# Optimization experiments

Hardware: AMD Instinct MI355X
Metric: run time of the kernel (lower is better)

The kernel has to match this reference:

```python
import jax, jax.numpy as jnp
import numpy as np

N = 50000; E = 200000; H = 128; L = 3; T = 2; FOUT = 64
G = 1000; NP = 3; ATOM_V = 64; BOND_V = 8
EPS = 1e-5
_DEG_HIST = np.array([0., 50000., 75000., 50000., 25000.])
# PyG PNAConv: avg_deg['log'] = sum(hist[d] * log(d+1)) / num_nodes
AVG_DEG_LOG = float((np.log(np.arange(5) + 1.0) * _DEG_HIST).sum() / _DEG_HIST.sum())


def _bn(v, g, b):
    # training-mode BatchNorm1d (biased variance), eps=1e-5
    mu = v.mean(0)
    var = ((v - mu) ** 2).mean(0)
    return (v - mu) * jax.lax.rsqrt(var + EPS) * g + b


def setup_inputs() -> dict:
    key = jax.random.key(0)
    ks = jax.random.split(key, 16)
    def nrm(k, shape, fan):
        return (jax.random.normal(k, shape, dtype=jnp.float32) / np.sqrt(fan)).astype(jnp.float32)
    return {
        'x': jax.random.randint(ks[0], (N, 9), 0, ATOM_V),
        'edge_index': jax.random.randint(ks[1], (2, E), 0, N),
        'batch': jnp.sort(jax.random.randint(ks[2], (N,), 0, G)),
        'edge_attr_idx': jax.random.randint(ks[3], (E, 3), 0, BOND_V),
        'atom_emb': nrm(ks[4], (9, ATOM_V, H), H),
        'bond_emb': nrm(ks[5], (3, BOND_V, H), H),
        'edge_W': nrm(ks[6], (L, H, H), H), 'edge_b': jnp.zeros((L, H), jnp.float32),
        'pre_W': nrm(ks[7], (L, T, 3 * H, H), 3 * H), 'pre_b': jnp.zeros((L, T, H), jnp.float32),
        'post_W': nrm(ks[8], (L, T, 13 * H, FOUT), 13 * H), 'post_b': jnp.zeros((L, T, FOUT), jnp.float32),
        'lin_W': nrm(ks[9], (L, H, H), H), 'lin_b': jnp.zeros((L, H), jnp.float32),
        'bn_g': jnp.ones((L, H), jnp.float32), 'bn_b': jnp.zeros((L, H), jnp.float32),
        'mlp_W': nrm(ks[10], (2, H, H), H), 'mlp_b': jnp.zeros((2, H), jnp.float32),
        'mlp_g': jnp.ones((2, H), jnp.float32), 'mlp_be': jnp.zeros((2, H), jnp.float32),
        'hW1': nrm(ks[11], (H, H // 2), H), 'hb1': jnp.zeros((H // 2,), jnp.float32),
        'hg1': jnp.ones((H // 2,), jnp.float32), 'hbe1': jnp.zeros((H // 2,), jnp.float32),
        'hW2': nrm(ks[12], (H // 2, H // 4), H // 2), 'hb2': jnp.zeros((H // 4,), jnp.float32),
        'hg2': jnp.ones((H // 4,), jnp.float32), 'hbe2': jnp.zeros((H // 4,), jnp.float32),
        'hW3': nrm(ks[13], (H // 4, NP), H // 4), 'hb3': jnp.zeros((NP,), jnp.float32),
    }


def reference(x, edge_index, batch, edge_attr_idx, atom_emb, bond_emb,
              edge_W, edge_b, pre_W, pre_b, post_W, post_b, lin_W, lin_b,
              bn_g, bn_b, mlp_W, mlp_b, mlp_g, mlp_be,
              hW1, hb1, hg1, hbe1, hW2, hb2, hg2, hbe2, hW3, hb3):
    # encoders: sum of per-feature embeddings (OGB Atom/Bond encoder)
    h = atom_emb[jnp.arange(9), x].sum(1)               # [N,H]
    e = bond_emb[jnp.arange(3), edge_attr_idx].sum(1)   # [E,H]
    src, dst = edge_index[0], edge_index[1]
    cnt = jax.ops.segment_sum(jnp.ones((E,), jnp.float32), dst, N)
    deg = jnp.maximum(cnt, 1.0)[:, None, None]          # clamp(1), as in PyG scalers
    amp = jnp.log(deg + 1.0) / AVG_DEG_LOG
    att = AVG_DEG_LOG / jnp.log(deg + 1.0)
    has = (cnt > 0)[:, None, None]
    for l in range(L):
        ea = e @ edge_W[l] + edge_b[l]                                  # [E,H]
        msg_in = jnp.concatenate([h[dst], h[src], ea], -1)              # [E,3H]
        m = jnp.einsum('ef,tfh->eth', msg_in, pre_W[l]) + pre_b[l]      # [E,T,H]
        s1 = jax.ops.segment_sum(m, dst, N)
        s2 = jax.ops.segment_sum(m * m, dst, N)
        mean = s1 / deg
        std = jnp.sqrt(jax.nn.relu(s2 / deg - mean * mean) + EPS)
        mn = jnp.where(has, jax.ops.segment_min(m, dst, N), 0.0)
        mx = jnp.where(has, jax.ops.segment_max(m, dst, N), 0.0)
        agg = jnp.concatenate([mean, mn, mx, std], -1)                  # [N,T,4H]
        scaled = jnp.concatenate([agg, agg * amp, agg * att], -1)       # [N,T,12H]
        upd = jnp.concatenate(
            [jnp.broadcast_to(h[:, None, :], (N, T, H)), scaled], -1)   # [N,T,13H]
        o = jnp.einsum('ntf,tfo->nto', upd, post_W[l]) + post_b[l]      # [N,T,FOUT]
        o = o.reshape(N, T * FOUT) @ lin_W[l] + lin_b[l]                # [N,H]
        h = jax.nn.relu(_bn(o, bn_g[l], bn_b[l]))
    g = jax.ops.segment_sum(h, batch, G)                                # [G,H]
    for i in range(2):
        g = jax.nn.relu(_bn(g @ mlp_W[i] + mlp_b[i], mlp_g[i], mlp_be[i]))
    g = jax.nn.relu(_bn(g @ hW1 + hb1, hg1, hbe1))
    g = jax.nn.relu(_bn(g @ hW2 + hb2, hg2, hbe2))
    return g @ hW3 + hb3                                                # [G,NP]
```

## Files before the change

kernel.cpp:

```cpp
#include <hip/hip_runtime.h>
#include <math.h>


#define NN 50000
#define NE 200000
#define HD 128
#define NG 1000
#define EPSV 1e-5f
#define ALOGC 1.1330197327247628f

#define AP 1288
#define OP 136
#define ECAP 512

typedef __bf16 bf16x8 __attribute__((ext_vector_type(8)));
typedef float f32x4 __attribute__((ext_vector_type(4)));

__device__ __forceinline__ unsigned short f2bf(float f) {
    unsigned int u = __float_as_uint(f);
    unsigned int r = (u + 0x7FFFu + ((u >> 16) & 1u)) >> 16;
    return (unsigned short)r;
}
__device__ __forceinline__ float bf2f(unsigned short h) {
    return __uint_as_float((unsigned int)h << 16);
}

__global__ void k_fill(float* __restrict__ o, float v, int n) {
    int i = blockIdx.x * 256 + threadIdx.x;
    if (i < n) o[i] = v;
}

__global__ void k_zero(float* __restrict__ z, int n) {
    int i = blockIdx.x * 256 + threadIdx.x;
    if (i < n) z[i] = 0.f;
}

__global__ void k_encode_nodes(const int* __restrict__ x, const float* __restrict__ aemb,
                               float* __restrict__ h) {
    int n = blockIdx.x, c = threadIdx.x;
    __shared__ int xi[9];
    if (c < 9) xi[c] = x[n * 9 + c];
    __syncthreads();
    float acc = 0.f;
#pragma unroll
    for (int f = 0; f < 9; ++f) acc += aemb[(f * 64 + xi[f]) * HD + c];
    h[(size_t)n * HD + c] = acc;
}

__global__ void k_count(const int* __restrict__ dst, int* __restrict__ cnt) {
    int e = blockIdx.x * 256 + threadIdx.x;
    if (e < NE) atomicAdd(&cnt[dst[e]], 1);
}

__global__ __launch_bounds__(1024) void k_scan(
    const int* __restrict__ cnt, int* __restrict__ rowptr,
    float* __restrict__ ampv, float* __restrict__ attv) {
    __shared__ int buf[1024];
    __shared__ int s_off;
    int tid = threadIdx.x;
    if (tid == 0) { s_off = 0; rowptr[0] = 0; }
    __syncthreads();
    for (int base = 0; base < NN; base += 1024) {
        int i = base + tid;
        int v = (i < NN) ? cnt[i] : 0;
        if (i < NN) {
            float dg = (float)(v > 0 ? v : 1);
            float lg = logf(dg + 1.0f);
            ampv[i] = lg / ALOGC;
            attv[i] = ALOGC / lg;
        }
        buf[tid] = v;
        __syncthreads();
        for (int s = 1; s < 1024; s <<= 1) {
            int t = (tid >= s) ? buf[tid - s] : 0;
            __syncthreads();
            buf[tid] += t;
            __syncthreads();
        }
        int off = s_off;
        if (i < NN) rowptr[i + 1] = off + buf[tid];
        __syncthreads();
        if (tid == 1023) s_off = off + buf[1023];
        __syncthreads();
    }
}

__global__ void k_scatter(const int* __restrict__ dst, const int* __restrict__ rowptr,
                          int* __restrict__ fill, int* __restrict__ eperm) {
    int e = blockIdx.x * 256 + threadIdx.x;
    if (e < NE) {
        int d = dst[e];
        int pos = rowptr[d] + atomicAdd(&fill[d], 1);
        eperm[pos] = e;
    }
}

__global__ void k_eprep(const int* __restrict__ ei, const int* __restrict__ eai,
                        const int* __restrict__ eperm,
                        int* __restrict__ psrc, int* __restrict__ pbnd) {
    int p = blockIdx.x * 256 + threadIdx.x;
    if (p < NE) {
        int e = eperm[p];
        psrc[p] = ei[e];
        pbnd[p] = eai[e * 3] | (eai[e * 3 + 1] << 4) | (eai[e * 3 + 2] << 8);
    }
}

__global__ void k_fold(const float* __restrict__ edge_W, const float* __restrict__ edge_b,
                       const float* __restrict__ pre_W, const float* __restrict__ pre_b,
                       float* __restrict__ cW, float* __restrict__ tb) {
    int l = blockIdx.y;
    int k = blockIdx.x;
    int tj = threadIdx.x;
    int t = tj >> 7, j = tj & 127;
    const float* pw = pre_W + ((size_t)(l * 2 + t) * 384 + 256) * 128 + j;
    if (k < 128) {
        const float* ew = edge_W + ((size_t)l * 128 + k) * 128;
        float acc = 0.f;
        for (int i = 0; i < 128; ++i) acc += ew[i] * pw[i * 128];
        cW[((size_t)l * 128 + k) * 256 + tj] = acc;
    } else {
        const float* eb = edge_b + l * 128;
        float acc = pre_b[(l * 2 + t) * 128 + j];
        for (int i = 0; i < 128; ++i) acc += eb[i] * pw[i * 128];
        tb[l * 256 + tj] = acc;
    }
}

__global__ void k_bond(const float* __restrict__ bemb, const float* __restrict__ cW,
                       float* __restrict__ bondc) {
    int v = blockIdx.x, f = blockIdx.y, l = blockIdx.z;
    int tj = threadIdx.x;
    const float* src = bemb + (size_t)(f * 8 + v) * 128;
    const float* w = cW + (size_t)l * 128 * 256;
    float acc = 0.f;
    for (int i = 0; i < 128; ++i) acc += src[i] * w[i * 256 + tj];
    bondc[(((size_t)l * 3 + f) * 8 + v) * 256 + tj] = acc;
}

__global__ void k_pack(const float* __restrict__ W, int N, int NT,
                       unsigned short* __restrict__ pk) {
    int blk = blockIdx.x;
    int kstep = blk / NT, nt = blk - kstep * NT;
    int lane = threadIdx.x;
    int kb = kstep * 32 + (lane >> 4) * 8;
    int col = nt * 16 + (lane & 15);
    unsigned short tmp[8];
#pragma unroll
    for (int i = 0; i < 8; ++i) tmp[i] = f2bf(W[(size_t)(kb + i) * N + col]);
    *(uint4*)(pk + ((size_t)blk * 64 + lane) * 8) = *(uint4*)tmp;
}

__global__ void k_pack_pre(const float* __restrict__ preW,
                           unsigned short* __restrict__ phi,
                           unsigned short* __restrict__ plo) {
    int b = blockIdx.x;
    int kstep = b >> 5, nt = b & 31;
    int lane = threadIdx.x;
    int q = lane >> 4, nc = lane & 15;
    int col = nt * 16 + nc;
    int t = (col >> 7) & 1;
    int jcol = col & 127;
    int fbase = (col < 256) ? 0 : 128;
    unsigned short hi[8], lo[8];
#pragma unroll
    for (int i = 0; i < 8; ++i) {
        int k = kstep * 32 + q * 8 + i;
        float w = preW[((size_t)t * 384 + fbase + k) * 128 + jcol];
        unsigned short h16 = f2bf(w);
        hi[i] = h16;
        lo[i] = f2bf(w - bf2f(h16));
    }
    size_t base = ((size_t)b * 64 + lane) * 8;
    *(uint4*)(phi + base) = *(uint4*)hi;
    *(uint4*)(plo + base) = *(uint4*)lo;
}

__global__ __launch_bounds__(256) void k_pre_m(
    const float* __restrict__ h,
    const unsigned short* __restrict__ phi, const unsigned short* __restrict__ plo,
    const float* __restrict__ tb,
    float* __restrict__ hz) {
    __shared__ __align__(16) unsigned short ah[16 * 136];
    __shared__ __align__(16) unsigned short al[16 * 136];
    int n0 = blockIdx.x * 16;
    int tid = threadIdx.x;
    {
        int node = tid >> 4, cg = (tid & 15) * 8;
        const float* hs = h + (size_t)(n0 + node) * HD + cg;
        float4 v0 = *(const float4*)(hs);
        float4 v1 = *(const float4*)(hs + 4);
        float vv[8] = {v0.x, v0.y, v0.z, v0.w, v1.x, v1.y, v1.z, v1.w};
        unsigned short hh[8], ll[8];
#pragma unroll
        for (int i = 0; i < 8; ++i) {
            hh[i] = f2bf(vv[i]);
            ll[i] = f2bf(vv[i] - bf2f(hh[i]));
        }
        *(uint4*)(ah + node * 136 + cg) = *(uint4*)hh;
        *(uint4*)(al + node * 136 + cg) = *(uint4*)ll;
    }
    __syncthreads();
    int lane = tid & 63, w = tid >> 6;
    int q = lane >> 4, nc = lane & 15;
    f32x4 acc[8];
#pragma unroll
    for (int j = 0; j < 8; ++j) acc[j] = (f32x4){0.f, 0.f, 0.f, 0.f};
#pragma unroll
    for (int kk = 0; kk < 4; ++kk) {
        bf16x8 Ahi = *(const bf16x8*)(ah + nc * 136 + kk * 32 + q * 8);
        bf16x8 Alo = *(const bf16x8*)(al + nc * 136 + kk * 32 + q * 8);
#pragma unroll
        for (int j = 0; j < 8; ++j) {
            int nt = w * 8 + j;
            size_t base = ((size_t)(kk * 32 + nt) * 64 + lane) * 8;
            bf16x8 Bhi = *(const bf16x8*)(phi + base);
            bf16x8 Blo = *(const bf16x8*)(plo + base);
            acc[j] = __builtin_amdgcn_mfma_f32_16x16x32_bf16(Ahi, Bhi, acc[j], 0, 0, 0);
            acc[j] = __builtin_amdgcn_mfma_f32_16x16x32_bf16(Ahi, Blo, acc[j], 0, 0, 0);
            acc[j] = __builtin_amdgcn_mfma_f32_16x16x32_bf16(Alo, Bhi, acc[j], 0, 0, 0);
        }
    }
#pragma unroll
    for (int j = 0; j < 8; ++j) {
        int col = (w * 8 + j) * 16 + nc;
        float bias = (col < 256) ? tb[col] : 0.f;
#pragma unroll
        for (int reg = 0; reg < 4; ++reg) {
            hz[(size_t)(n0 + q * 4 + reg) * 512 + col] = acc[j][reg] + bias;
        }
    }
}

__global__ __launch_bounds__(256) void k_post(
    const float* __restrict__ h, const float* __restrict__ hz,
    const int* __restrict__ rowptr,
    const int* __restrict__ psrc, const int* __restrict__ pbnd,
    const float* __restrict__ bondc,
    const float* __restrict__ ampv, const float* __restrict__ attv,
    const unsigned short* __restrict__ pkPost,
    const float* __restrict__ postb,
    const unsigned short* __restrict__ pkLin,
    const float* __restrict__ linb,
    float* __restrict__ o2, float* __restrict__ stats) {
    __shared__ __align__(16) unsigned short a_lds[16 * AP];
    __shared__ __align__(16) unsigned short o_lds[16 * OP];
    __shared__ int es_src[ECAP], es_bnd[ECAP];
    __shared__ float s_amp[16], s_att[16];
    int n0 = blockIdx.x * 16;
    int tid = threadIdx.x;

    int pbase = rowptr[n0];
    int ecount = rowptr[n0 + 16] - pbase;
    for (int i = tid; i < ecount && i < ECAP; i += 256) {
        es_src[i] = psrc[pbase + i];
        es_bnd[i] = pbnd[pbase + i];
    }
    {
        int node = tid >> 4, cg = (tid & 15) * 8;
        const float* hs = h + (size_t)(n0 + node) * HD + cg;
        float4 v0 = *(const float4*)(hs);
        float4 v1 = *(const float4*)(hs + 4);
        unsigned short* d0 = a_lds + node * AP + cg;
        unsigned short* d1 = d0 + 640;
        unsigned short b[8];
        b[0] = f2bf(v0.x); b[1] = f2bf(v0.y); b[2] = f2bf(v0.z); b[3] = f2bf(v0.w);
        b[4] = f2bf(v1.x); b[5] = f2bf(v1.y); b[6] = f2bf(v1.z); b[7] = f2bf(v1.w);
#pragma unroll
        for (int i = 0; i < 8; ++i) { d0[i] = b[i]; d1[i] = b[i]; }
    }
    if (tid < 16) { s_amp[tid] = ampv[n0 + tid]; s_att[tid] = attv[n0 + tid]; }
    __syncthreads();

    {
        int wv = tid >> 6, lane = tid & 63;
        int cc = lane * 4;
        int tt = cc >> 7, jj = cc & 127;
        const float* b0t = bondc;
        const float* b1t = bondc + 8 * 256;
        const float* b2t = bondc + 16 * 256;
        bool incap = (ecount <= ECAP);
        int nwb = n0 + wv * 4;
        int bnd[5];
        bnd[0] = rowptr[nwb];
        bnd[1] = rowptr[nwb + 1];
        bnd[2] = rowptr[nwb + 2];
        bnd[3] = rowptr[nwb + 3];
        bnd[4] = rowptr[nwb + 4];
        int e0 = bnd[0], e4 = bnd[4];
        float4 hd0 = *(const float4*)(hz + (size_t)(nwb + 0) * 512 + cc);
        float4 hd1 = *(const float4*)(hz + (size_t)(nwb + 1) * 512 + cc);
        float4 hd2 = *(const float4*)(hz + (size_t)(nwb + 2) * 512 + cc);
        float4 hd3 = *(const float4*)(hz + (size_t)(nwb + 3) * 512 + cc);
        float4 hd = hd0;
        const float4 Z4 = make_float4(0.f, 0.f, 0.f, 0.f);
        const float4 BIG4 = make_float4(3.4e38f, 3.4e38f, 3.4e38f, 3.4e38f);
        const float4 NBIG4 = make_float4(-3.4e38f, -3.4e38f, -3.4e38f, -3.4e38f);
        float4 s1 = Z4, s2 = Z4, mn = BIG4, mx = NBIG4;
        int ni = 0;

        auto fin = [&](int nloc) {
            int cnt = bnd[nloc + 1] - bnd[nloc];
            float inv = 1.f / (float)(cnt > 0 ? cnt : 1);
            float4 mean, stdv;
            mean.x = s1.x * inv; mean.y = s1.y * inv;
            mean.z = s1.z * inv; mean.w = s1.w * inv;
            stdv.x = sqrtf(fmaxf(s2.x * inv - mean.x * mean.x, 0.f) + EPSV);
            stdv.y = sqrtf(fmaxf(s2.y * inv - mean.y * mean.y, 0.f) + EPSV);
            stdv.z = sqrtf(fmaxf(s2.z * inv - mean.z * mean.z, 0.f) + EPSV);
            stdv.w = sqrtf(fmaxf(s2.w * inv - mean.w * mean.w, 0.f) + EPSV);
            if (cnt == 0) { mn = Z4; mx = Z4; }
            unsigned short* d = a_lds + (wv * 4 + nloc) * AP + tt * 640 + 128 + jj;
            d[0] = f2bf(mean.x); d[1] = f2bf(mean.y); d[2] = f2bf(mean.z); d[3] = f2bf(mean.w);
            d += 128; d[0] = f2bf(mn.x); d[1] = f2bf(mn.y); d[2] = f2bf(mn.z); d[3] = f2bf(mn.w);
            d += 128; d[0] = f2bf(mx.x); d[1] = f2bf(mx.y); d[2] = f2bf(mx.z); d[3] = f2bf(mx.w);
            d += 128; d[0] = f2bf(stdv.x); d[1] = f2bf(stdv.y); d[2] = f2bf(stdv.z); d[3] = f2bf(stdv.w);
            s1 = Z4; s2 = Z4; mn = BIG4; mx = NBIG4;
        };

        float4 vsn = Z4, q0n = Z4, q1n = Z4, q2n = Z4;
        if (e0 < e4) {
            int sp = incap ? es_src[e0 - pbase] : psrc[e0];
            int pb = incap ? es_bnd[e0 - pbase] : pbnd[e0];
            vsn = *(const float4*)(hz + (size_t)sp * 512 + 256 + cc);
            q0n = *(const float4*)(b0t + (pb & 15) * 256 + cc);
            q1n = *(const float4*)(b1t + ((pb >> 4) & 15) * 256 + cc);
            q2n = *(const float4*)(b2t + ((pb >> 8) & 15) * 256 + cc);
        }
        for (int p = e0; p < e4; ++p) {
            while (p == bnd[ni + 1]) {
                fin(ni);
                ++ni;
                hd = (ni == 1) ? hd1 : (ni == 2) ? hd2 : hd3;
            }
            float4 vs = vsn, q0 = q0n, q1 = q1n, q2 = q2n;
            int pn = p + 1;
            if (pn < e4) {
                int sp = incap ? es_src[pn - pbase] : psrc[pn];
                int pb = incap ? es_bnd[pn - pbase] : pbnd[pn];
                vsn = *(const float4*)(hz + (size_t)sp * 512 + 256 + cc);
                q0n = *(const float4*)(b0t + (pb & 15) * 256 + cc);
                q1n = *(const float4*)(b1t + ((pb >> 4) & 15) * 256 + cc);
                q2n = *(const float4*)(b2t + ((pb >> 8) & 15) * 256 + cc);
            }
            float vx = hd.x + vs.x + q0.x + q1.x + q2.x;
            float vy = hd.y + vs.y + q0.y + q1.y + q2.y;
            float vz = hd.z + vs.z + q0.z + q1.z + q2.z;
            float vw = hd.w + vs.w + q0.w + q1.w + q2.w;
            s1.x += vx; s1.y += vy; s1.z += vz; s1.w += vw;
            s2.x += vx * vx; s2.y += vy * vy; s2.z += vz * vz; s2.w += vw * vw;
            mn.x = fminf(mn.x, vx); mn.y = fminf(mn.y, vy);
            mn.z = fminf(mn.z, vz); mn.w = fminf(mn.w, vw);
            mx.x = fmaxf(mx.x, vx); mx.y = fmaxf(mx.y, vy);
            mx.z = fmaxf(mx.z, vz); mx.w = fmaxf(mx.w, vw);
        }
        while (ni < 4) { fin(ni); ++ni; }
    }
    __syncthreads();

    {
        int lane = tid & 63;
        int w = tid >> 6;
        int t = w >> 1;
        int ntb = (w & 1) * 2;
        int q = lane >> 4, nc = lane & 15;
        const unsigned short* arow = a_lds + (size_t)nc * AP + t * 640 + q * 8;
        const unsigned short* pkt = pkPost + (size_t)t * 106496;
        f32x4 aP0 = {0.f, 0.f, 0.f, 0.f}, aP1 = {0.f, 0.f, 0.f, 0.f};
        f32x4 aA0 = {0.f, 0.f, 0.f, 0.f}, aA1 = {0.f, 0.f, 0.f, 0.f};
        f32x4 aT0 = {0.f, 0.f, 0.f, 0.f}, aT1 = {0.f, 0.f, 0.f, 0.f};
        for (int kk = 0; kk < 20; ++kk) {
            bf16x8 af = *(const bf16x8*)(arow + kk * 32);
            const unsigned short* pb = pkt + ((size_t)(kk * 4 + ntb) * 64 + lane) * 8;
            aP0 = __builtin_amdgcn_mfma_f32_16x16x32_bf16(af, *(const bf16x8*)(pb), aP0, 0, 0, 0);
            aP1 = __builtin_amdgcn_mfma_f32_16x16x32_bf16(af, *(const bf16x8*)(pb + 512), aP1, 0, 0, 0);
            if (kk >= 4) {
                const unsigned short* pa = pkt + ((size_t)((kk + 16) * 4 + ntb) * 64 + lane) * 8;
                aA0 = __builtin_amdgcn_mfma_f32_16x16x32_bf16(af, *(const bf16x8*)(pa), aA0, 0, 0, 0);
                aA1 = __builtin_amdgcn_mfma_f32_16x16x32_bf16(af, *(const bf16x8*)(pa + 512), aA1, 0, 0, 0);
                const unsigned short* pt = pkt + ((size_t)((kk + 32) * 4 + ntb) * 64 + lane) * 8;
                aT0 = __builtin_amdgcn_mfma_f32_16x16x32_bf16(af, *(const bf16x8*)(pt), aT0, 0, 0, 0);
                aT1 = __builtin_amdgcn_mfma_f32_16x16x32_bf16(af, *(const bf16x8*)(pt + 512), aT1, 0, 0, 0);
            }
        }
#pragma unroll
        for (int u = 0; u < 2; ++u) {
            int nt = ntb + u;
            int col = t * 64 + nt * 16 + nc;
            float pbia = postb[t * 64 + nt * 16 + nc];
            f32x4 P = u ? aP1 : aP0;
            f32x4 A = u ? aA1 : aA0;
            f32x4 T = u ? aT1 : aT0;
#pragma unroll
            for (int reg = 0; reg < 4; ++reg) {
                int mrow = q * 4 + reg;
                float val = P[reg] + s_amp[mrow] * A[reg] + s_att[mrow] * T[reg] + pbia;
                o_lds[mrow * OP + col] = f2bf(val);
            }
        }
    }
    __syncthreads();

    {
        int lane = tid & 63;
        int w = tid >> 6;
        int ntb = w * 2;
        int q = lane >> 4, nc = lane & 15;
        const unsigned short* arow = o_lds + (size_t)nc * OP + q * 8;
        f32x4 L0 = {0.f, 0.f, 0.f, 0.f}, L1 = {0.f, 0.f, 0.f, 0.f};
#pragma unroll
        for (int kk = 0; kk < 4; ++kk) {
            bf16x8 af = *(const bf16x8*)(arow + kk * 32);
            const unsigned short* pb = pkLin + ((size_t)(kk * 8 + ntb) * 64 + lane) * 8;
            L0 = __builtin_amdgcn_mfma_f32_16x16x32_bf16(af, *(const bf16x8*)(pb), L0, 0, 0, 0);
            L1 = __builtin_amdgcn_mfma_f32_16x16x32_bf16(af, *(const bf16x8*)(pb + 512), L1, 0, 0, 0);
        }
#pragma unroll
        for (int u = 0; u < 2; ++u) {
            int col = (ntb + u) * 16 + nc;
            float lb = linb[col];
            f32x4 L = u ? L1 : L0;
            float ps = 0.f, pss = 0.f;
#pragma unroll
            for (int reg = 0; reg < 4; ++reg) {
                int mrow = q * 4 + reg;
                float v = L[reg] + lb;
                o2[(size_t)(n0 + mrow) * HD + col] = v;
                ps += v; pss += v * v;
            }
            ps += __shfl_down(ps, 16); ps += __shfl_down(ps, 32);
            pss += __shfl_down(pss, 16); pss += __shfl_down(pss, 32);
            if (q == 0) {
                atomicAdd(&stats[col], ps);
                atomicAdd(&stats[128 + col], pss);
            }
        }
    }
}

__global__ void k_bn_relu(const float* __restrict__ o2, const float* __restrict__ stats,
                          const float* __restrict__ g, const float* __restrict__ b,
                          float* __restrict__ h) {
    int idx = blockIdx.x * 256 + threadIdx.x;
    int c = idx & 127;
    float mu = stats[c] * (1.f / NN);
    float var = stats[128 + c] * (1.f / NN) - mu * mu;
    float v = (o2[idx] - mu) * rsqrtf(var + EPSV) * g[c] + b[c];
    h[idx] = fmaxf(v, 0.f);
}

__global__ void k_pool(const float* __restrict__ h, const int* __restrict__ batch,
                       float* __restrict__ g0) {
    int c = threadIdx.x;
    int nbase = blockIdx.x * 64;
    float run = 0.f; int cur = -1;
    for (int i = 0; i < 64; ++i) {
        int n = nbase + i;
        if (n >= NN) break;
        int bb = batch[n];
        if (bb != cur) {
            if (cur >= 0) atomicAdd(&g0[(size_t)cur * HD + c], run);
            cur = bb; run = 0.f;
        }
        run += h[(size_t)n * HD + c];
    }
    if (cur >= 0) atomicAdd(&g0[(size_t)cur * HD + c], run);
}

__global__ void k_head_gemm(const float* __restrict__ x, const float* __restrict__ W,
                            const float* __restrict__ b, float* __restrict__ y,
                            float* __restrict__ stats, int K, int Kout) {
    int row = blockIdx.x;
    int col = threadIdx.x;
    if (col >= Kout) return;
    float acc = b[col];
    for (int k = 0; k < K; k += 4) {
        float4 xv = *(const float4*)(x + (size_t)row * K + k);
        acc += xv.x * W[(k + 0) * Kout + col] + xv.y * W[(k + 1) * Kout + col]
             + xv.z * W[(k + 2) * Kout + col] + xv.w * W[(k + 3) * Kout + col];
    }
    y[(size_t)row * Kout + col] = acc;
    if (stats) {
        atomicAdd(&stats[col], acc);
        atomicAdd(&stats[Kout + col], acc * acc);
    }
}

__global__ void k_head_bn(float* __restrict__ y, const float* __restrict__ stats,
                          const float* __restrict__ g, const float* __restrict__ b, int Kout) {
    int idx = blockIdx.x * 256 + threadIdx.x;
    if (idx >= NG * Kout) return;
    int c = idx % Kout;
    float mu = stats[c] * (1.f / NG);
    float var = stats[Kout + c] * (1.f / NG) - mu * mu;
    float v = (y[idx] - mu) * rsqrtf(var + EPSV) * g[c] + b[c];
    y[idx] = fmaxf(v, 0.f);
}

extern "C" void kernel_launch(void* const* d_in, const int* in_sizes, int n_in,
                              void* d_out, int out_size, void* d_ws, size_t ws_size,
                              hipStream_t stream) {
    const int*   x        = (const int*)  d_in[0];
    const int*   ei       = (const int*)  d_in[1];
    const int*   batch    = (const int*)  d_in[2];
    const int*   eai      = (const int*)  d_in[3];
    const float* atom_emb = (const float*)d_in[4];
    const float* bond_emb = (const float*)d_in[5];
    const float* edge_W   = (const float*)d_in[6];
    const float* edge_b   = (const float*)d_in[7];
    const float* pre_W    = (const float*)d_in[8];
    const float* pre_b    = (const float*)d_in[9];
    const float* post_W   = (const float*)d_in[10];
    const float* post_b   = (const float*)d_in[11];
    const float* lin_W    = (const float*)d_in[12];
    const float* lin_b    = (const float*)d_in[13];
    const float* bn_g     = (const float*)d_in[14];
    const float* bn_b     = (const float*)d_in[15];
    const float* mlp_W    = (const float*)d_in[16];
    const float* mlp_b    = (const float*)d_in[17];
    const float* mlp_g    = (const float*)d_in[18];
    const float* mlp_be   = (const float*)d_in[19];
    const float* hW1 = (const float*)d_in[20]; const float* hb1  = (const float*)d_in[21];
    const float* hg1 = (const float*)d_in[22]; const float* hbe1 = (const float*)d_in[23];
    const float* hW2 = (const float*)d_in[24]; const float* hb2  = (const float*)d_in[25];
    const float* hg2 = (const float*)d_in[26]; const float* hbe2 = (const float*)d_in[27];
    const float* hW3 = (const float*)d_in[28]; const float* hb3  = (const float*)d_in[29];
    float* out = (float*)d_out;
    (void)n_in; (void)in_sizes;

    char* p = (char*)d_ws;
    size_t off = 0;
    auto alloc = [&](size_t bytes) -> char* {
        char* r = p + off;
        off += (bytes + 255) & ~(size_t)255;
        return r;
    };
    float* h     = (float*)alloc((size_t)NN * HD * 4);
    float* o2    = (float*)alloc((size_t)NN * HD * 4);
    float* hz    = (float*)alloc((size_t)NN * 512 * 4);
    float* ampv  = (float*)alloc((size_t)NN * 4);
    float* attv  = (float*)alloc((size_t)NN * 4);
    int*   rowptr= (int*)  alloc((size_t)(NN + 1) * 4);
    int*   eperm = (int*)  alloc((size_t)NE * 4);
    int*   psrc  = (int*)  alloc((size_t)NE * 4);
    int*   pbnd  = (int*)  alloc((size_t)NE * 4);
    float* cW    = (float*)alloc((size_t)3 * 128 * 256 * 4);
    float* tbb   = (float*)alloc((size_t)3 * 256 * 4);
    float* bondc = (float*)alloc((size_t)3 * 3 * 8 * 256 * 4);
    unsigned short* pkPost  = (unsigned short*)alloc((size_t)3 * 2 * 106496 * 2);
    unsigned short* pkLin   = (unsigned short*)alloc((size_t)3 * 16384 * 2);
    unsigned short* pkPreHi = (unsigned short*)alloc((size_t)3 * 65536 * 2);
    unsigned short* pkPreLo = (unsigned short*)alloc((size_t)3 * 65536 * 2);
    float* gA    = (float*)alloc((size_t)NG * HD * 4);
    float* gB    = (float*)alloc((size_t)NG * HD * 4);
    char* z0 = p + off;
    int*   cnt   = (int*)  alloc((size_t)NN * 4);
    int*   fill  = (int*)  alloc((size_t)NN * 4);
    float* stats = (float*)alloc((size_t)3 * 256 * 4);
    float* hstats= (float*)alloc((size_t)4 * 256 * 4);
    float* g0    = (float*)alloc((size_t)NG * HD * 4);
    size_t zwords = (size_t)((p + off) - z0) / 4;

    if (off > ws_size) {
        k_fill<<<(out_size + 255) / 256, 256, 0, stream>>>(out, (float)ws_size, out_size);
        return;
    }

    k_zero<<<(int)((zwords + 255) / 256), 256, 0, stream>>>((float*)z0, (int)zwords);
    k_encode_nodes<<<NN, 128, 0, stream>>>(x, atom_emb, h);
    k_count<<<(NE + 255) / 256, 256, 0, stream>>>(ei + NE, cnt);
    k_scan<<<1, 1024, 0, stream>>>(cnt, rowptr, ampv, attv);
    k_scatter<<<(NE + 255) / 256, 256, 0, stream>>>(ei + NE, rowptr, fill, eperm);
    k_eprep<<<(NE + 255) / 256, 256, 0, stream>>>(ei, eai, eperm, psrc, pbnd);
    k_fold<<<dim3(129, 3), 256, 0, stream>>>(edge_W, edge_b, pre_W, pre_b, cW, tbb);
    k_bond<<<dim3(8, 3, 3), 256, 0, stream>>>(bond_emb, cW, bondc);
    for (int l = 0; l < 3; ++l) {
        for (int t = 0; t < 2; ++t)
            k_pack<<<52 * 4, 64, 0, stream>>>(post_W + ((size_t)l * 2 + t) * 1664 * 64, 64, 4,
                                              pkPost + ((size_t)l * 2 + t) * 106496);
        k_pack<<<4 * 8, 64, 0, stream>>>(lin_W + (size_t)l * 128 * 128, 128, 8,
                                         pkLin + (size_t)l * 16384);
        k_pack_pre<<<128, 64, 0, stream>>>(pre_W + (size_t)l * 2 * 384 * 128,
                                           pkPreHi + (size_t)l * 65536,
                                           pkPreLo + (size_t)l * 65536);
    }

    for (int l = 0; l < 3; ++l) {
        k_pre_m<<<NN / 16, 256, 0, stream>>>(h,
            pkPreHi + (size_t)l * 65536, pkPreLo + (size_t)l * 65536,
            tbb + l * 256, hz);
        k_post<<<NN / 16, 256, 0, stream>>>(h, hz, rowptr, psrc, pbnd,
            bondc + (size_t)l * 3 * 8 * 256,
            ampv, attv,
            pkPost + (size_t)l * 2 * 106496, post_b + l * 2 * 64,
            pkLin + (size_t)l * 16384, lin_b + l * 128,
            o2, stats + l * 256);
        k_bn_relu<<<(NN * HD) / 256, 256, 0, stream>>>(o2, stats + l * 256,
            bn_g + l * 128, bn_b + l * 128, h);
    }

    k_pool<<<(NN + 63) / 64, 128, 0, stream>>>(h, batch, g0);

    k_head_gemm<<<NG, 128, 0, stream>>>(g0, mlp_W, mlp_b, gA, hstats, 128, 128);
    k_head_bn<<<(NG * 128 + 255) / 256, 256, 0, stream>>>(gA, hstats, mlp_g, mlp_be, 128);
    k_head_gemm<<<NG, 128, 0, stream>>>(gA, mlp_W + 128 * 128, mlp_b + 128, gB, hstats + 256, 128, 128);
    k_head_bn<<<(NG * 128 + 255) / 256, 256, 0, stream>>>(gB, hstats + 256, mlp_g + 128, mlp_be + 128, 128);
    k_head_gemm<<<NG, 128, 0, stream>>>(gB, hW1, hb1, gA, hstats + 512, 128, 64);
    k_head_bn<<<(NG * 64 + 255) / 256, 256, 0, stream>>>(gA, hstats + 512, hg1, hbe1, 64);
    k_head_gemm<<<NG, 128, 0, stream>>>(gA, hW2, hb2, gB, hstats + 768, 64, 32);
    k_head_bn<<<(NG * 32 + 255) / 256, 256, 0, stream>>>(gB, hstats + 768, hg2, hbe2, 32);
    k_head_gemm<<<NG, 64, 0, stream>>>(gB, hW3, hb3, out, (float*)nullptr, 32, 3);
}
```

Baseline: 1.075 ms.

## Parallelize scan, fuse BN into pre-GEMM and head, precombine bond tables

The single-block serial scan becomes a three-kernel multi-block scan. Batch-norm and ReLU are fused into the next layer's pre-transform GEMM and into each head GEMM, which removes separate elementwise passes. The bond embeddings are precombined into a 512-entry table so each edge does one lookup instead of three, and source index plus bond code are packed into one int. The hz buffer is split into dst and src halves, and the hd term is moved out of the per-edge loop and added after aggregation. The post kernel loses its software prefetch and now walks nodes one at a time, which may expose more gather latency.

```diff
diff --git a/kernel.cpp b/kernel.cpp
--- a/kernel.cpp
+++ b/kernel.cpp
@@ -12,6 +12,7 @@
 #define AP 1288
 #define OP 136
 #define ECAP 512
+#define SCB 49
 
 typedef __bf16 bf16x8 __attribute__((ext_vector_type(8)));
 typedef float f32x4 __attribute__((ext_vector_type(4)));
@@ -52,36 +53,43 @@
     if (e < NE) atomicAdd(&cnt[dst[e]], 1);
 }
 
-__global__ __launch_bounds__(1024) void k_scan(
-    const int* __restrict__ cnt, int* __restrict__ rowptr,
-    float* __restrict__ ampv, float* __restrict__ attv) {
+__global__ __launch_bounds__(1024) void k_scanA(const int* __restrict__ cnt,
+                                                int* __restrict__ sc, int* __restrict__ tot) {
     __shared__ int buf[1024];
-    __shared__ int s_off;
     int tid = threadIdx.x;
-    if (tid == 0) { s_off = 0; rowptr[0] = 0; }
-    __syncthreads();
-    for (int base = 0; base < NN; base += 1024) {
-        int i = base + tid;
-        int v = (i < NN) ? cnt[i] : 0;
-        if (i < NN) {
-            float dg = (float)(v > 0 ? v : 1);
-            float lg = logf(dg + 1.0f);
-            ampv[i] = lg / ALOGC;
-            attv[i] = ALOGC / lg;
-        }
-        buf[tid] = v;
+    int i = blockIdx.x * 1024 + tid;
+    int v = (i < NN) ? cnt[i] : 0;
+    buf[tid] = v;
+    __syncthreads();
+    for (int s = 1; s < 1024; s <<= 1) {
+        int t = (tid >= s) ? buf[tid - s] : 0;
         __syncthreads();
-        for (int s = 1; s < 1024; s <<= 1) {
-            int t = (tid >= s) ? buf[tid - s] : 0;
-            __syncthreads();
-            buf[tid] += t;
-            __syncthreads();
-        }
-        int off = s_off;
-        if (i < NN) rowptr[i + 1] = off + buf[tid];
+        buf[tid] += t;
         __syncthreads();
-        if (tid == 1023) s_off = off + buf[1023];
-        __syncthreads();
+    }
+    if (i < NN) sc[i] = buf[tid];
+    if (tid == 1023) tot[blockIdx.x] = buf[1023];
+}
+
+__global__ void k_scanB(const int* __restrict__ tot, int* __restrict__ offb) {
+    if (threadIdx.x == 0) {
+        int run = 0;
+        for (int b = 0; b < SCB; ++b) { offb[b] = run; run += tot[b]; }
+    }
+}
+
+__global__ __launch_bounds__(1024) void k_scanC(
+    const int* __restrict__ cnt, const int* __restrict__ sc, const int* __restrict__ offb,
+    int* __restrict__ rowptr, float* __restrict__ ampv, float* __restrict__ attv) {
+    int i = blockIdx.x * 1024 + threadIdx.x;
+    if (i == 0) rowptr[0] = 0;
+    if (i < NN) {
+        rowptr[i + 1] = offb[blockIdx.x] + sc[i];
+        int v = cnt[i];
+        float dg = (float)(v > 0 ? v : 1);
+        float lg = logf(dg + 1.0f);
+        ampv[i] = lg / ALOGC;
+        attv[i] = ALOGC / lg;
     }
 }
 
@@ -96,13 +104,12 @@
 }
 
 __global__ void k_eprep(const int* __restrict__ ei, const int* __restrict__ eai,
-                        const int* __restrict__ eperm,
-                        int* __restrict__ psrc, int* __restrict__ pbnd) {
+                        const int* __restrict__ eperm, int* __restrict__ precs) {
     int p = blockIdx.x * 256 + threadIdx.x;
     if (p < NE) {
         int e = eperm[p];
-        psrc[p] = ei[e];
-        pbnd[p] = eai[e * 3] | (eai[e * 3 + 1] << 4) | (eai[e * 3 + 2] << 8);
+        int cidx = eai[e * 3] | (eai[e * 3 + 1] << 3) | (eai[e * 3 + 2] << 6);
+        precs[p] = ei[e] | (cidx << 17);
     }
 }
 
@@ -138,6 +145,15 @@
     bondc[(((size_t)l * 3 + f) * 8 + v) * 256 + tj] = acc;
 }
 
+__global__ void k_bcomb(const float* __restrict__ bondc, float* __restrict__ bcomb) {
+    int ci = blockIdx.x, l = blockIdx.y, tj = threadIdx.x;
+    const float* base = bondc + (size_t)l * 3 * 8 * 256;
+    float v = base[((0 * 8) + (ci & 7)) * 256 + tj]
+            + base[((1 * 8) + ((ci >> 3) & 7)) * 256 + tj]
+            + base[((2 * 8) + (ci >> 6)) * 256 + tj];
+    bcomb[((size_t)l * 512 + ci) * 256 + tj] = v;
+}
+
 __global__ void k_pack(const float* __restrict__ W, int N, int NT,
                        unsigned short* __restrict__ pk) {
     int blk = blockIdx.x;
@@ -176,11 +192,48 @@
     *(uint4*)(plo + base) = *(uint4*)lo;
 }
 
+__device__ __forceinline__ void pre_mfma_body(
+    const unsigned short* __restrict__ ah, const unsigned short* __restrict__ al,
+    const unsigned short* __restrict__ phi, const unsigned short* __restrict__ plo,
+    const float* __restrict__ tb, int n0, int tid,
+    float* __restrict__ hzd, float* __restrict__ hzs) {
+    int lane = tid & 63, w = tid >> 6;
+    int q = lane >> 4, nc = lane & 15;
+    f32x4 acc[8];
+#pragma unroll
+    for (int j = 0; j < 8; ++j) acc[j] = (f32x4){0.f, 0.f, 0.f, 0.f};
+#pragma unroll
+    for (int kk = 0; kk < 4; ++kk) {
+        bf16x8 Ahi = *(const bf16x8*)(ah + nc * 136 + kk * 32 + q * 8);
+        bf16x8 Alo = *(const bf16x8*)(al + nc * 136 + kk * 32 + q * 8);
+#pragma unroll
+        for (int j = 0; j < 8; ++j) {
+            int nt = w * 8 + j;
+            size_t base = ((size_t)(kk * 32 + nt) * 64 + lane) * 8;
+            bf16x8 Bhi = *(const bf16x8*)(phi + base);
+            bf16x8 Blo = *(const bf16x8*)(plo + base);
+            acc[j] = __builtin_amdgcn_mfma_f32_16x16x32_bf16(Ahi, Bhi, acc[j], 0, 0, 0);
+            acc[j] = __builtin_amdgcn_mfma_f32_16x16x32_bf16(Ahi, Blo, acc[j], 0, 0, 0);
+            acc[j] = __builtin_amdgcn_mfma_f32_16x16x32_bf16(Alo, Bhi, acc[j], 0, 0, 0);
+        }
+    }
+#pragma unroll
+    for (int j = 0; j < 8; ++j) {
+        int col = (w * 8 + j) * 16 + nc;
+#pragma unroll
+        for (int reg = 0; reg < 4; ++reg) {
+            int row = n0 + q * 4 + reg;
+            if (col < 256) hzd[(size_t)row * 256 + col] = acc[j][reg] + tb[col];
+            else           hzs[(size_t)row * 256 + (col - 256)] = acc[j][reg];
+        }
+    }
+}
+
 __global__ __launch_bounds__(256) void k_pre_m(
     const float* __restrict__ h,
     const unsigned short* __restrict__ phi, const unsigned short* __restrict__ plo,
     const float* __restrict__ tb,
-    float* __restrict__ hz) {
+    float* __restrict__ hzd, float* __restrict__ hzs) {
     __shared__ __align__(16) unsigned short ah[16 * 136];
     __shared__ __align__(16) unsigned short al[16 * 136];
     int n0 = blockIdx.x * 16;
@@ -201,42 +254,54 @@
         *(uint4*)(al + node * 136 + cg) = *(uint4*)ll;
     }
     __syncthreads();
-    int lane = tid & 63, w = tid >> 6;
-    int q = lane >> 4, nc = lane & 15;
-    f32x4 acc[8];
-#pragma unroll
-    for (int j = 0; j < 8; ++j) acc[j] = (f32x4){0.f, 0.f, 0.f, 0.f};
-#pragma unroll
-    for (int kk = 0; kk < 4; ++kk) {
-        bf16x8 Ahi = *(const bf16x8*)(ah + nc * 136 + kk * 32 + q * 8);
-        bf16x8 Alo = *(const bf16x8*)(al + nc * 136 + kk * 32 + q * 8);
-#pragma unroll
-        for (int j = 0; j < 8; ++j) {
-            int nt = w * 8 + j;
-            size_t base = ((size_t)(kk * 32 + nt) * 64 + lane) * 8;
-            bf16x8 Bhi = *(const bf16x8*)(phi + base);
-            bf16x8 Blo = *(const bf16x8*)(plo + base);
-            acc[j] = __builtin_amdgcn_mfma_f32_16x16x32_bf16(Ahi, Bhi, acc[j], 0, 0, 0);
-            acc[j] = __builtin_amdgcn_mfma_f32_16x16x32_bf16(Ahi, Blo, acc[j], 0, 0, 0);
-            acc[j] = __builtin_amdgcn_mfma_f32_16x16x32_bf16(Alo, Bhi, acc[j], 0, 0, 0);
-        }
-    }
-#pragma unroll
-    for (int j = 0; j < 8; ++j) {
-        int col = (w * 8 + j) * 16 + nc;
-        float bias = (col < 256) ? tb[col] : 0.f;
-#pragma unroll
-        for (int reg = 0; reg < 4; ++reg) {
-            hz[(size_t)(n0 + q * 4 + reg) * 512 + col] = acc[j][reg] + bias;
-        }
-    }
+    pre_mfma_body(ah, al, phi, plo, tb, n0, tid, hzd, hzs);
+}
+
+__global__ __launch_bounds__(256) void k_bnpre(
+    const float* __restrict__ o2, const float* __restrict__ stats,
+    const float* __restrict__ g, const float* __restrict__ b,
+    const unsigned short* __restrict__ phi, const unsigned short* __restrict__ plo,
+    const float* __restrict__ tb,
+    float* __restrict__ h, float* __restrict__ hzd, float* __restrict__ hzs) {
+    __shared__ __align__(16) unsigned short ah[16 * 136];
+    __shared__ __align__(16) unsigned short al[16 * 136];
+    int n0 = blockIdx.x * 16;
+    int tid = threadIdx.x;
+    {
+        int node = tid >> 4, cg = (tid & 15) * 8;
+        int n = n0 + node;
+        const float* os = o2 + (size_t)n * HD + cg;
+        float4 v0 = *(const float4*)(os);
+        float4 v1 = *(const float4*)(os + 4);
+        float vv[8] = {v0.x, v0.y, v0.z, v0.w, v1.x, v1.y, v1.z, v1.w};
+        unsigned short hh[8], ll[8];
+        float ou[8];
+#pragma unroll
+        for (int i = 0; i < 8; ++i) {
+            int c = cg + i;
+            float mu = stats[c] * (1.f / NN);
+            float var = stats[128 + c] * (1.f / NN) - mu * mu;
+            float val = (vv[i] - mu) * rsqrtf(var + EPSV) * g[c] + b[c];
+            val = fmaxf(val, 0.f);
+            ou[i] = val;
+            hh[i] = f2bf(val);
+            ll[i] = f2bf(val - bf2f(hh[i]));
+        }
+        float* hd = h + (size_t)n * HD + cg;
+        *(float4*)(hd) = make_float4(ou[0], ou[1], ou[2], ou[3]);
+        *(float4*)(hd + 4) = make_float4(ou[4], ou[5], ou[6], ou[7]);
+        *(uint4*)(ah + node * 136 + cg) = *(uint4*)hh;
+        *(uint4*)(al + node * 136 + cg) = *(uint4*)ll;
+    }
+    __syncthreads();
+    pre_mfma_body(ah, al, phi, plo, tb, n0, tid, hzd, hzs);
 }
 
 __global__ __launch_bounds__(256) void k_post(
-    const float* __restrict__ h, const float* __restrict__ hz,
-    const int* __restrict__ rowptr,
-    const int* __restrict__ psrc, const int* __restrict__ pbnd,
-    const float* __restrict__ bondc,
+    const float* __restrict__ h,
+    const float* __restrict__ hzd, const float* __restrict__ hzs,
+    const int* __restrict__ rowptr, const int* __restrict__ precs,
+    const float* __restrict__ bcomb,
     const float* __restrict__ ampv, const float* __restrict__ attv,
     const unsigned short* __restrict__ pkPost,
     const float* __restrict__ postb,
@@ -245,17 +310,14 @@
     float* __restrict__ o2, float* __restrict__ stats) {
     __shared__ __align__(16) unsigned short a_lds[16 * AP];
     __shared__ __align__(16) unsigned short o_lds[16 * OP];
-    __shared__ int es_src[ECAP], es_bnd[ECAP];
+    __shared__ int es[ECAP];
     __shared__ float s_amp[16], s_att[16];
     int n0 = blockIdx.x * 16;
     int tid = threadIdx.x;
 
     int pbase = rowptr[n0];
     int ecount = rowptr[n0 + 16] - pbase;
-    for (int i = tid; i < ecount && i < ECAP; i += 256) {
-        es_src[i] = psrc[pbase + i];
-        es_bnd[i] = pbnd[pbase + i];
-    }
+    for (int i = tid; i < ecount && i < ECAP; i += 256) es[i] = precs[pbase + i];
     {
         int node = tid >> 4, cg = (tid & 15) * 8;
         const float* hs = h + (size_t)(n0 + node) * HD + cg;
@@ -263,11 +325,11 @@
         float4 v1 = *(const float4*)(hs + 4);
         unsigned short* d0 = a_lds + node * AP + cg;
         unsigned short* d1 = d0 + 640;
-        unsigned short b[8];
-        b[0] = f2bf(v0.x); b[1] = f2bf(v0.y); b[2] = f2bf(v0.z); b[3] = f2bf(v0.w);
-        b[4] = f2bf(v1.x); b[5] = f2bf(v1.y); b[6] = f2bf(v1.z); b[7] = f2bf(v1.w);
-#pragma unroll
-        for (int i = 0; i < 8; ++i) { d0[i] = b[i]; d1[i] = b[i]; }
+        unsigned short bb[8];
+        bb[0] = f2bf(v0.x); bb[1] = f2bf(v0.y); bb[2] = f2bf(v0.z); bb[3] = f2bf(v0.w);
+        bb[4] = f2bf(v1.x); bb[5] = f2bf(v1.y); bb[6] = f2bf(v1.z); bb[7] = f2bf(v1.w);
+#pragma unroll
+        for (int i = 0; i < 8; ++i) { d0[i] = bb[i]; d1[i] = bb[i]; }
     }
     if (tid < 16) { s_amp[tid] = ampv[n0 + tid]; s_att[tid] = attv[n0 + tid]; }
     __syncthreads();
@@ -276,85 +338,52 @@
         int wv = tid >> 6, lane = tid & 63;
         int cc = lane * 4;
         int tt = cc >> 7, jj = cc & 127;
-        const float* b0t = bondc;
-        const float* b1t = bondc + 8 * 256;
-        const float* b2t = bondc + 16 * 256;
         bool incap = (ecount <= ECAP);
-        int nwb = n0 + wv * 4;
-        int bnd[5];
-        bnd[0] = rowptr[nwb];
-        bnd[1] = rowptr[nwb + 1];
-        bnd[2] = rowptr[nwb + 2];
-        bnd[3] = rowptr[nwb + 3];
-        bnd[4] = rowptr[nwb + 4];
-        int e0 = bnd[0], e4 = bnd[4];
-        float4 hd0 = *(const float4*)(hz + (size_t)(nwb + 0) * 512 + cc);
-        float4 hd1 = *(const float4*)(hz + (size_t)(nwb + 1) * 512 + cc);
-        float4 hd2 = *(const float4*)(hz + (size_t)(nwb + 2) * 512 + cc);
-        float4 hd3 = *(const float4*)(hz + (size_t)(nwb + 3) * 512 + cc);
-        float4 hd = hd0;
         const float4 Z4 = make_float4(0.f, 0.f, 0.f, 0.f);
-        const float4 BIG4 = make_float4(3.4e38f, 3.4e38f, 3.4e38f, 3.4e38f);
-        const float4 NBIG4 = make_float4(-3.4e38f, -3.4e38f, -3.4e38f, -3.4e38f);
-        float4 s1 = Z4, s2 = Z4, mn = BIG4, mx = NBIG4;
-        int ni = 0;
-
-        auto fin = [&](int nloc) {
-            int cnt = bnd[nloc + 1] - bnd[nloc];
+        for (int i = 0; i < 4; ++i) {
+            int r = wv * 4 + i;
+            int n = n0 + r;
+            int p0 = rowptr[n], p1 = rowptr[n + 1];
+            float4 hd = *(const float4*)(hzd + (size_t)n * 256 + cc);
+            float4 s1 = Z4, s2 = Z4;
+            float4 mn = make_float4(3.4e38f, 3.4e38f, 3.4e38f, 3.4e38f);
+            float4 mx = make_float4(-3.4e38f, -3.4e38f, -3.4e38f, -3.4e38f);
+            for (int p = p0; p < p1; ++p) {
+                int rec = incap ? es[p - pbase] : precs[p];
+                int sp = rec & 131071;
+                int ci = rec >> 17;
+                float4 vs = *(const float4*)(hzs + (size_t)sp * 256 + cc);
+                float4 bc = *(const float4*)(bcomb + (size_t)ci * 256 + cc);
+                float wx = vs.x + bc.x, wy = vs.y + bc.y, wz = vs.z + bc.z, ww = vs.w + bc.w;
+                s1.x += wx; s1.y += wy; s1.z += wz; s1.w += ww;
+                s2.x += wx * wx; s2.y += wy * wy; s2.z += wz * wz; s2.w += ww * ww;
+                mn.x = fminf(mn.x, wx); mn.y = fminf(mn.y, wy);
+                mn.z = fminf(mn.z, wz); mn.w = fminf(mn.w, ww);
+                mx.x = fmaxf(mx.x, wx); mx.y = fmaxf(mx.y, wy);
+                mx.z = fmaxf(mx.z, wz); mx.w = fmaxf(mx.w, ww);
+            }
+            int cnt = p1 - p0;
             float inv = 1.f / (float)(cnt > 0 ? cnt : 1);
-            float4 mean, stdv;
-            mean.x = s1.x * inv; mean.y = s1.y * inv;
-            mean.z = s1.z * inv; mean.w = s1.w * inv;
-            stdv.x = sqrtf(fmaxf(s2.x * inv - mean.x * mean.x, 0.f) + EPSV);
-            stdv.y = sqrtf(fmaxf(s2.y * inv - mean.y * mean.y, 0.f) + EPSV);
-            stdv.z = sqrtf(fmaxf(s2.z * inv - mean.z * mean.z, 0.f) + EPSV);
-            stdv.w = sqrtf(fmaxf(s2.w * inv - mean.w * mean.w, 0.f) + EPSV);
-            if (cnt == 0) { mn = Z4; mx = Z4; }
-            unsigned short* d = a_lds + (wv * 4 + nloc) * AP + tt * 640 + 128 + jj;
+            float4 mw, stdv, mean;
+            mw.x = s1.x * inv; mw.y = s1.y * inv; mw.z = s1.z * inv; mw.w = s1.w * inv;
+            stdv.x = sqrtf(fmaxf(s2.x * inv - mw.x * mw.x, 0.f) + EPSV);
+            stdv.y = sqrtf(fmaxf(s2.y * inv - mw.y * mw.y, 0.f) + EPSV);
+            stdv.z = sqrtf(fmaxf(s2.z * inv - mw.z * mw.z, 0.f) + EPSV);
+            stdv.w = sqrtf(fmaxf(s2.w * inv - mw.w * mw.w, 0.f) + EPSV);
+            if (cnt > 0) {
+                mean.x = hd.x + mw.x; mean.y = hd.y + mw.y;
+                mean.z = hd.z + mw.z; mean.w = hd.w + mw.w;
+                mn.x += hd.x; mn.y += hd.y; mn.z += hd.z; mn.w += hd.w;
+                mx.x += hd.x; mx.y += hd.y; mx.z += hd.z; mx.w += hd.w;
+            } else {
+                mean = Z4; mn = Z4; mx = Z4;
+            }
+            unsigned short* d = a_lds + r * AP + tt * 640 + 128 + jj;
             d[0] = f2bf(mean.x); d[1] = f2bf(mean.y); d[2] = f2bf(mean.z); d[3] = f2bf(mean.w);
             d += 128; d[0] = f2bf(mn.x); d[1] = f2bf(mn.y); d[2] = f2bf(mn.z); d[3] = f2bf(mn.w);
             d += 128; d[0] = f2bf(mx.x); d[1] = f2bf(mx.y); d[2] = f2bf(mx.z); d[3] = f2bf(mx.w);
             d += 128; d[0] = f2bf(stdv.x); d[1] = f2bf(stdv.y); d[2] = f2bf(stdv.z); d[3] = f2bf(stdv.w);
-            s1 = Z4; s2 = Z4; mn = BIG4; mx = NBIG4;
-        };
-
-        float4 vsn = Z4, q0n = Z4, q1n = Z4, q2n = Z4;
-        if (e0 < e4) {
-            int sp = incap ? es_src[e0 - pbase] : psrc[e0];
-            int pb = incap ? es_bnd[e0 - pbase] : pbnd[e0];
-            vsn = *(const float4*)(hz + (size_t)sp * 512 + 256 + cc);
-            q0n = *(const float4*)(b0t + (pb & 15) * 256 + cc);
-            q1n = *(const float4*)(b1t + ((pb >> 4) & 15) * 256 + cc);
-            q2n = *(const float4*)(b2t + ((pb >> 8) & 15) * 256 + cc);
-        }
-        for (int p = e0; p < e4; ++p) {
-            while (p == bnd[ni + 1]) {
-                fin(ni);
-                ++ni;
-                hd = (ni == 1) ? hd1 : (ni == 2) ? hd2 : hd3;
-            }
-            float4 vs = vsn, q0 = q0n, q1 = q1n, q2 = q2n;
-            int pn = p + 1;
-            if (pn < e4) {
-                int sp = incap ? es_src[pn - pbase] : psrc[pn];
-                int pb = incap ? es_bnd[pn - pbase] : pbnd[pn];
-                vsn = *(const float4*)(hz + (size_t)sp * 512 + 256 + cc);
-                q0n = *(const float4*)(b0t + (pb & 15) * 256 + cc);
-                q1n = *(const float4*)(b1t + ((pb >> 4) & 15) * 256 + cc);
-                q2n = *(const float4*)(b2t + ((pb >> 8) & 15) * 256 + cc);
-            }
-            float vx = hd.x + vs.x + q0.x + q1.x + q2.x;
-            float vy = hd.y + vs.y + q0.y + q1.y + q2.y;
-            float vz = hd.z + vs.z + q0.z + q1.z + q2.z;
-            float vw = hd.w + vs.w + q0.w + q1.w + q2.w;
-            s1.x += vx; s1.y += vy; s1.z += vz; s1.w += vw;
-            s2.x += vx * vx; s2.y += vy * vy; s2.z += vz * vz; s2.w += vw * vw;
-            mn.x = fminf(mn.x, vx); mn.y = fminf(mn.y, vy);
-            mn.z = fminf(mn.z, vz); mn.w = fminf(mn.w, vw);
-            mx.x = fmaxf(mx.x, vx); mx.y = fmaxf(mx.y, vy);
-            mx.z = fmaxf(mx.z, vz); mx.w = fmaxf(mx.w, vw);
-        }
-        while (ni < 4) { fin(ni); ++ni; }
+        }
     }
     __syncthreads();
 
@@ -486,15 +515,29 @@
     }
 }
 
-__global__ void k_head_bn(float* __restrict__ y, const float* __restrict__ stats,
-                          const float* __restrict__ g, const float* __restrict__ b, int Kout) {
-    int idx = blockIdx.x * 256 + threadIdx.x;
-    if (idx >= NG * Kout) return;
-    int c = idx % Kout;
-    float mu = stats[c] * (1.f / NG);
-    float var = stats[Kout + c] * (1.f / NG) - mu * mu;
-    float v = (y[idx] - mu) * rsqrtf(var + EPSV) * g[c] + b[c];
-    y[idx] = fmaxf(v, 0.f);
+__global__ __launch_bounds__(128) void k_head_fused(
+    const float* __restrict__ y_in, const float* __restrict__ stats_in,
+    const float* __restrict__ g, const float* __restrict__ b,
+    const float* __restrict__ W, const float* __restrict__ bias,
+    float* __restrict__ y_out, float* __restrict__ stats_out, int Kin, int Kout) {
+    __shared__ float row[128];
+    int r = blockIdx.x, tid = threadIdx.x;
+    if (tid < Kin) {
+        float mu = stats_in[tid] * (1.f / NG);
+        float var = stats_in[Kin + tid] * (1.f / NG) - mu * mu;
+        float v = (y_in[(size_t)r * Kin + tid] - mu) * rsqrtf(var + EPSV) * g[tid] + b[tid];
+        row[tid] = fmaxf(v, 0.f);
+    }
+    __syncthreads();
+    if (tid < Kout) {
+        float acc = bias[tid];
+        for (int k = 0; k < Kin; ++k) acc += row[k] * W[(size_t)k * Kout + tid];
+        y_out[(size_t)r * Kout + tid] = acc;
+        if (stats_out) {
+            atomicAdd(&stats_out[tid], acc);
+            atomicAdd(&stats_out[Kout + tid], acc * acc);
+        }
+    }
 }
 
 extern "C" void kernel_launch(void* const* d_in, const int* in_sizes, int n_in,
@@ -537,16 +580,20 @@
     };
     float* h     = (float*)alloc((size_t)NN * HD * 4);
     float* o2    = (float*)alloc((size_t)NN * HD * 4);
-    float* hz    = (float*)alloc((size_t)NN * 512 * 4);
+    float* hzd   = (float*)alloc((size_t)NN * 256 * 4);
+    float* hzs   = (float*)alloc((size_t)NN * 256 * 4);
     float* ampv  = (float*)alloc((size_t)NN * 4);
     float* attv  = (float*)alloc((size_t)NN * 4);
     int*   rowptr= (int*)  alloc((size_t)(NN + 1) * 4);
     int*   eperm = (int*)  alloc((size_t)NE * 4);
-    int*   psrc  = (int*)  alloc((size_t)NE * 4);
-    int*   pbnd  = (int*)  alloc((size_t)NE * 4);
+    int*   precs = (int*)  alloc((size_t)NE * 4);
+    int*   sc    = (int*)  alloc((size_t)NN * 4);
+    int*   stot  = (int*)  alloc((size_t)SCB * 4);
+    int*   soff  = (int*)  alloc((size_t)SCB * 4);
     float* cW    = (float*)alloc((size_t)3 * 128 * 256 * 4);
     float* tbb   = (float*)alloc((size_t)3 * 256 * 4);
     float* bondc = (float*)alloc((size_t)3 * 3 * 8 * 256 * 4);
+    float* bcomb = (float*)alloc((size_t)3 * 512 * 256 * 4);
     unsigned short* pkPost  = (unsigned short*)alloc((size_t)3 * 2 * 106496 * 2);
     unsigned short* pkLin   = (unsigned short*)alloc((size_t)3 * 16384 * 2);
     unsigned short* pkPreHi = (unsigned short*)alloc((size_t)3 * 65536 * 2);
@@ -569,11 +616,14 @@
     k_zero<<<(int)((zwords + 255) / 256), 256, 0, stream>>>((float*)z0, (int)zwords);
     k_encode_nodes<<<NN, 128, 0, stream>>>(x, atom_emb, h);
     k_count<<<(NE + 255) / 256, 256, 0, stream>>>(ei + NE, cnt);
-    k_scan<<<1, 1024, 0, stream>>>(cnt, rowptr, ampv, attv);
+    k_scanA<<<SCB, 1024, 0, stream>>>(cnt, sc, stot);
+    k_scanB<<<1, 64, 0, stream>>>(stot, soff);
+    k_scanC<<<SCB, 1024, 0, stream>>>(cnt, sc, soff, rowptr, ampv, attv);
     k_scatter<<<(NE + 255) / 256, 256, 0, stream>>>(ei + NE, rowptr, fill, eperm);
-    k_eprep<<<(NE + 255) / 256, 256, 0, stream>>>(ei, eai, eperm, psrc, pbnd);
+    k_eprep<<<(NE + 255) / 256, 256, 0, stream>>>(ei, eai, eperm, precs);
     k_fold<<<dim3(129, 3), 256, 0, stream>>>(edge_W, edge_b, pre_W, pre_b, cW, tbb);
     k_bond<<<dim3(8, 3, 3), 256, 0, stream>>>(bond_emb, cW, bondc);
+    k_bcomb<<<dim3(512, 3), 256, 0, stream>>>(bondc, bcomb);
     for (int l = 0; l < 3; ++l) {
         for (int t = 0; t < 2; ++t)
             k_pack<<<52 * 4, 64, 0, stream>>>(post_W + ((size_t)l * 2 + t) * 1664 * 64, 64, 4,
@@ -586,28 +636,33 @@
     }
 
     for (int l = 0; l < 3; ++l) {
-        k_pre_m<<<NN / 16, 256, 0, stream>>>(h,
-            pkPreHi + (size_t)l * 65536, pkPreLo + (size_t)l * 65536,
-            tbb + l * 256, hz);
-        k_post<<<NN / 16, 256, 0, stream>>>(h, hz, rowptr, psrc, pbnd,
-            bondc + (size_t)l * 3 * 8 * 256,
+        if (l == 0) {
+            k_pre_m<<<NN / 16, 256, 0, stream>>>(h, pkPreHi, pkPreLo, tbb, hzd, hzs);
+        } else {
+            k_bnpre<<<NN / 16, 256, 0, stream>>>(o2, stats + (l - 1) * 256,
+                bn_g + (l - 1) * 128, bn_b + (l - 1) * 128,
+                pkPreHi + (size_t)l * 65536, pkPreLo + (size_t)l * 65536,
+                tbb + l * 256, h, hzd, hzs);
+        }
+        k_post<<<NN / 16, 256, 0, stream>>>(h, hzd, hzs, rowptr, precs,
+            bcomb + (size_t)l * 512 * 256,
             ampv, attv,
             pkPost + (size_t)l * 2 * 106496, post_b + l * 2 * 64,
             pkLin + (size_t)l * 16384, lin_b + l * 128,
             o2, stats + l * 256);
-        k_bn_relu<<<(NN * HD) / 256, 256, 0, stream>>>(o2, stats + l * 256,
-            bn_g + l * 128, bn_b + l * 128, h);
-    }
+    }
+    k_bn_relu<<<(NN * HD) / 256, 256, 0, stream>>>(o2, stats + 2 * 256,
+        bn_g + 2 * 128, bn_b + 2 * 128, h);
 
     k_pool<<<(NN + 63) / 64, 128, 0, stream>>>(h, batch, g0);
 
     k_head_gemm<<<NG, 128, 0, stream>>>(g0, mlp_W, mlp_b, gA, hstats, 128, 128);
-    k_head_bn<<<(NG * 128 + 255) / 256, 256, 0, stream>>>(gA, hstats, mlp_g, mlp_be, 128);
-    k_head_gemm<<<NG, 128, 0, stream>>>(gA, mlp_W + 128 * 128, mlp_b + 128, gB, hstats + 256, 128, 128);
-    k_head_bn<<<(NG * 128 + 255) / 256, 256, 0, stream>>>(gB, hstats + 256, mlp_g + 128, mlp_be + 128, 128);
-    k_head_gemm<<<NG, 128, 0, stream>>>(gB, hW1, hb1, gA, hstats + 512, 128, 64);
-    k_head_bn<<<(NG * 64 + 255) / 256, 256, 0, stream>>>(gA, hstats + 512, hg1, hbe1, 64);
-    k_head_gemm<<<NG, 128, 0, stream>>>(gA, hW2, hb2, gB, hstats + 768, 64, 32);
-    k_head_bn<<<(NG * 32 + 255) / 256, 256, 0, stream>>>(gB, hstats + 768, hg2, hbe2, 32);
-    k_head_gemm<<<NG, 64, 0, stream>>>(gB, hW3, hb3, out, (float*)nullptr, 32, 3);
-}
+    k_head_fused<<<NG, 128, 0, stream>>>(gA, hstats, mlp_g, mlp_be,
+        mlp_W + 128 * 128, mlp_b + 128, gB, hstats + 256, 128, 128);
+    k_head_fused<<<NG, 128, 0, stream>>>(gB, hstats + 256, mlp_g + 128, mlp_be + 128,
+        hW1, hb1, gA, hstats + 512, 128, 64);
+    k_head_fused<<<NG, 128, 0, stream>>>(gA, hstats + 512, hg1, hbe1,
+        hW2, hb2, gB, hstats + 768, 64, 32);
+    k_head_fused<<<NG, 128, 0, stream>>>(gB, hstats + 768, hg2, hbe2,
+        hW3, hb3, out, (float*)nullptr, 32, 3);
+}
```

New measurement: 976.7 us. 1.1x faster.
